# Performance work log

Hardware: AMD Instinct MI355X
Metric: run time of the kernel (lower is better)

The kernel has to match this reference:

```python
import jax, jax.numpy as jnp
import numpy as np

N_RAYS = 65536
N_SAMPLES = 4194304  # ~64 samples per ray, packed
D = 8


def setup_inputs() -> dict:
    key = jax.random.key(0)
    k1, k2 = jax.random.split(key)
    sample_values = jax.random.normal(k1, (N_SAMPLES, D), dtype=jnp.float32)
    ray_indices = jnp.sort(jax.random.randint(k2, (N_SAMPLES,), 0, N_RAYS, dtype=jnp.int32))
    return {"sample_values": sample_values, "ray_indices": ray_indices, "n_rays": N_RAYS}


def reference(sample_values, ray_indices, n_rays):
    # Segment-sum over variable-length per-ray sample packs.
    values_sum_per_ray = jax.ops.segment_sum(
        sample_values, ray_indices, num_segments=n_rays, indices_are_sorted=True
    )  # [n_rays, D]
    # Each sample receives its ray's total sum (gather back).
    values_sum_per_sample = values_sum_per_ray[ray_indices]  # [n_samples, D]
    return (values_sum_per_ray, values_sum_per_sample)
```

## Files before the change

### kernel.cpp

```cpp
#include <hip/hip_runtime.h>


#define DCH 8
#define RPW 8

typedef float f32x4 __attribute__((ext_vector_type(4)));

__global__ void __launch_bounds__(256) bounds_kernel(
    const int* __restrict__ rays,
    int* __restrict__ seg_start,
    int* __restrict__ seg_end,
    int n_samples, int n_rays) {
  long i = (long)blockIdx.x * blockDim.x + threadIdx.x;
  if (i >= n_samples) return;
  int r = rays[i];
  if (i == 0) {
    seg_start[r] = 0;
    for (int g = 0; g < r; ++g) { seg_start[g] = 0; seg_end[g] = 0; }
  } else {
    int rp = rays[i - 1];
    if (rp != r) {
      seg_end[rp] = (int)i;
      seg_start[r] = (int)i;
      for (int g = rp + 1; g < r; ++g) { seg_start[g] = (int)i; seg_end[g] = (int)i; }
    }
  }
  if (i == n_samples - 1) {
    seg_end[r] = n_samples;
    for (int g = r + 1; g < n_rays; ++g) { seg_start[g] = n_samples; seg_end[g] = n_samples; }
  }
}

__global__ void __launch_bounds__(256) raysum_kernel(
    const f32x4* __restrict__ vals4,
    const int* __restrict__ seg_start,
    const int* __restrict__ seg_end,
    f32x4* __restrict__ out_ray4,
    f32x4* __restrict__ out_sample4,
    int n_rays) {
  const int wave = blockIdx.x * (blockDim.x >> 6) + (threadIdx.x >> 6);
  const int base = wave * RPW;
  if (base >= n_rays) return;
  const int lane = threadIdx.x & 63;
  const int sl = lane >> 1;
  const int h = lane & 1;

  const int ridx = base + (lane & (RPW - 1));
  int rs = 0, re = 0;
  if (ridx < n_rays) {
    rs = seg_start[ridx];
    re = seg_end[ridx];
  }

#pragma unroll 1
  for (int r = 0; r < RPW; ++r) {
    if (base + r >= n_rays) break;
    const int s0 = __shfl(rs, r, 64);
    const int s1 = __shfl(re, r, 64);

    f32x4 acc = {0.f, 0.f, 0.f, 0.f};
    for (int j = s0 + sl; j < s1; j += 32) {
      f32x4 v = vals4[(long)j * 2 + h];
      acc += v;
    }

#pragma unroll
    for (int off = 2; off <= 32; off <<= 1) {
      acc.x += __shfl_xor(acc.x, off, 64);
      acc.y += __shfl_xor(acc.y, off, 64);
      acc.z += __shfl_xor(acc.z, off, 64);
      acc.w += __shfl_xor(acc.w, off, 64);
    }

    if (lane < 2) {
      out_ray4[(long)(base + r) * 2 + lane] = acc;
    }

    for (int j = s0 + sl; j < s1; j += 32) {
      __builtin_nontemporal_store(acc, &out_sample4[(long)j * 2 + h]);
    }
  }
}

extern "C" void kernel_launch(void* const* d_in, const int* in_sizes, int n_in,
                              void* d_out, int out_size, void* d_ws, size_t ws_size,
                              hipStream_t stream) {
  const float* vals = (const float*)d_in[0];
  const int* rays   = (const int*)d_in[1];

  const int n_samples = in_sizes[1];
  const int d         = in_sizes[0] / n_samples;
  const int n_rays    = out_size / d - n_samples;

  float* out_ray    = (float*)d_out;
  float* out_sample = out_ray + (size_t)n_rays * d;

  int* seg_start = (int*)d_ws;
  int* seg_end   = seg_start + n_rays;

  bounds_kernel<<<(int)(((long)n_samples + 255) / 256), 256, 0, stream>>>(
      rays, seg_start, seg_end, n_samples, n_rays);

  const int nwaves = (n_rays + RPW - 1) / RPW;
  const int nblocks = (nwaves + 3) / 4;
  raysum_kernel<<<nblocks, 256, 0, stream>>>(
      reinterpret_cast<const f32x4*>(vals), seg_start, seg_end,
      reinterpret_cast<f32x4*>(out_ray),
      reinterpret_cast<f32x4*>(out_sample), n_rays);
}
```

Measured before the change: 274.0 us.

## Batch rays per wave and prefetch first sample windows to raise memory parallelism

Each wave now handles its rays in two batches of four. For every ray it issues the first three strided loads up front, clamped and masked so they never fall out of bounds, before any reduction starts. This puts many independent loads in flight instead of looping one ray at a time with dependent accumulation. The per-sample writes also switch from nontemporal to ordinary stores. The cost is higher register pressure from the 24 prefetched vectors, possible wasted loads on short segments, and a change in cache behaviour from dropping the nontemporal stores.

```diff
diff --git a/kernel.cpp b/kernel.cpp
--- a/kernel.cpp
+++ b/kernel.cpp
@@ -3,6 +3,7 @@
 
 #define DCH 8
 #define RPW 8
+#define BATCH 4
 
 typedef float f32x4 __attribute__((ext_vector_type(4)));
 
@@ -31,19 +32,28 @@
   }
 }
 
+__device__ __forceinline__ f32x4 loadw(const f32x4* __restrict__ vals4,
+                                       long j, int s1, int nsm1, int h) {
+  long jc = j < (long)nsm1 ? j : (long)nsm1;
+  f32x4 v = vals4[jc * 2 + h];
+  f32x4 z = {0.f, 0.f, 0.f, 0.f};
+  return (j < (long)s1) ? v : z;
+}
+
 __global__ void __launch_bounds__(256) raysum_kernel(
     const f32x4* __restrict__ vals4,
     const int* __restrict__ seg_start,
     const int* __restrict__ seg_end,
     f32x4* __restrict__ out_ray4,
     f32x4* __restrict__ out_sample4,
-    int n_rays) {
+    int n_rays, int n_samples) {
   const int wave = blockIdx.x * (blockDim.x >> 6) + (threadIdx.x >> 6);
   const int base = wave * RPW;
   if (base >= n_rays) return;
   const int lane = threadIdx.x & 63;
   const int sl = lane >> 1;
   const int h = lane & 1;
+  const int nsm1 = n_samples - 1;
 
   const int ridx = base + (lane & (RPW - 1));
   int rs = 0, re = 0;
@@ -52,33 +62,81 @@
     re = seg_end[ridx];
   }
 
-#pragma unroll 1
-  for (int r = 0; r < RPW; ++r) {
-    if (base + r >= n_rays) break;
-    const int s0 = __shfl(rs, r, 64);
-    const int s1 = __shfl(re, r, 64);
+  int a0[BATCH], a1[BATCH], b0[BATCH], b1[BATCH];
+#pragma unroll
+  for (int q = 0; q < BATCH; ++q) {
+    a0[q] = __shfl(rs, q, 64);
+    a1[q] = __shfl(re, q, 64);
+    b0[q] = __shfl(rs, BATCH + q, 64);
+    b1[q] = __shfl(re, BATCH + q, 64);
+  }
 
-    f32x4 acc = {0.f, 0.f, 0.f, 0.f};
-    for (int j = s0 + sl; j < s1; j += 32) {
-      f32x4 v = vals4[(long)j * 2 + h];
-      acc += v;
-    }
+  f32x4 wa[BATCH][3], wb[BATCH][3];
+#pragma unroll
+  for (int q = 0; q < BATCH; ++q)
+#pragma unroll
+    for (int k = 0; k < 3; ++k)
+      wa[q][k] = loadw(vals4, (long)a0[q] + 32 * k + sl, a1[q], nsm1, h);
+#pragma unroll
+  for (int q = 0; q < BATCH; ++q)
+#pragma unroll
+    for (int k = 0; k < 3; ++k)
+      wb[q][k] = loadw(vals4, (long)b0[q] + 32 * k + sl, b1[q], nsm1, h);
 
+  {
+    f32x4 acc[BATCH];
+#pragma unroll
+    for (int q = 0; q < BATCH; ++q) acc[q] = wa[q][0] + wa[q][1] + wa[q][2];
+#pragma unroll
+    for (int q = 0; q < BATCH; ++q)
+      for (long j = (long)a0[q] + 96 + sl; j < a1[q]; j += 32)
+        acc[q] += vals4[j * 2 + h];
 #pragma unroll
     for (int off = 2; off <= 32; off <<= 1) {
-      acc.x += __shfl_xor(acc.x, off, 64);
-      acc.y += __shfl_xor(acc.y, off, 64);
-      acc.z += __shfl_xor(acc.z, off, 64);
-      acc.w += __shfl_xor(acc.w, off, 64);
+#pragma unroll
+      for (int q = 0; q < BATCH; ++q) {
+        acc[q].x += __shfl_xor(acc[q].x, off, 64);
+        acc[q].y += __shfl_xor(acc[q].y, off, 64);
+        acc[q].z += __shfl_xor(acc[q].z, off, 64);
+        acc[q].w += __shfl_xor(acc[q].w, off, 64);
+      }
     }
+#pragma unroll
+    for (int q = 0; q < BATCH; ++q)
+      if (lane < 2 && base + q < n_rays)
+        out_ray4[(long)(base + q) * 2 + lane] = acc[q];
+#pragma unroll
+    for (int q = 0; q < BATCH; ++q)
+      for (long j = (long)a0[q] + sl; j < a1[q]; j += 32)
+        out_sample4[j * 2 + h] = acc[q];
+  }
 
-    if (lane < 2) {
-      out_ray4[(long)(base + r) * 2 + lane] = acc;
+  {
+    f32x4 acc[BATCH];
+#pragma unroll
+    for (int q = 0; q < BATCH; ++q) acc[q] = wb[q][0] + wb[q][1] + wb[q][2];
+#pragma unroll
+    for (int q = 0; q < BATCH; ++q)
+      for (long j = (long)b0[q] + 96 + sl; j < b1[q]; j += 32)
+        acc[q] += vals4[j * 2 + h];
+#pragma unroll
+    for (int off = 2; off <= 32; off <<= 1) {
+#pragma unroll
+      for (int q = 0; q < BATCH; ++q) {
+        acc[q].x += __shfl_xor(acc[q].x, off, 64);
+        acc[q].y += __shfl_xor(acc[q].y, off, 64);
+        acc[q].z += __shfl_xor(acc[q].z, off, 64);
+        acc[q].w += __shfl_xor(acc[q].w, off, 64);
+      }
     }
-
-    for (int j = s0 + sl; j < s1; j += 32) {
-      __builtin_nontemporal_store(acc, &out_sample4[(long)j * 2 + h]);
-    }
+#pragma unroll
+    for (int q = 0; q < BATCH; ++q)
+      if (lane < 2 && base + BATCH + q < n_rays)
+        out_ray4[(long)(base + BATCH + q) * 2 + lane] = acc[q];
+#pragma unroll
+    for (int q = 0; q < BATCH; ++q)
+      for (long j = (long)b0[q] + sl; j < b1[q]; j += 32)
+        out_sample4[j * 2 + h] = acc[q];
   }
 }
 
@@ -106,5 +164,5 @@
   raysum_kernel<<<nblocks, 256, 0, stream>>>(
       reinterpret_cast<const f32x4*>(vals), seg_start, seg_end,
       reinterpret_cast<f32x4*>(out_ray),
-      reinterpret_cast<f32x4*>(out_sample), n_rays);
+      reinterpret_cast<f32x4*>(out_sample), n_rays, n_samples);
 }
```

Result: faster. 258.4 us (-5.7%).
